# Kernel tuning notes

Measured on AMD Instinct MI355X. Metric: run time of the kernel, lower is better.

Reference implementation:

```python
import jax, jax.numpy as jnp
import numpy as np

N = 100000      # nodes
E = 1600000     # edges (avg degree 16)
IN, H, OUT = 128, 128, 64


def setup_inputs() -> dict:
    key = jax.random.key(0)
    ks = jax.random.split(key, 6)
    x = jax.random.normal(ks[0], (N, IN), dtype=jnp.float32)
    edge_index = jax.random.randint(ks[1], (2, E), 0, N, dtype=jnp.int64)
    # normalize=False => adj_t values hold precomputed GCN norm weights
    edge_weight = jax.random.uniform(ks[2], (E,), dtype=jnp.float32)

    def glorot(k, fi, fo):
        lim = np.sqrt(6.0 / (fi + fo)).astype(np.float32)
        return jax.random.uniform(k, (fi, fo), jnp.float32, -lim, lim)

    W1, b1 = glorot(ks[3], IN, H), jnp.zeros((H,), jnp.float32)
    W2, b2 = glorot(ks[4], H, H), jnp.zeros((H,), jnp.float32)
    W3, b3 = glorot(ks[5], H, OUT), jnp.zeros((OUT,), jnp.float32)
    return {"x": x, "edge_index": edge_index, "edge_weight": edge_weight,
            "W1": W1, "b1": b1, "W2": W2, "b2": b2, "W3": W3, "b3": b3}


def _gcn_conv(x, W, b, src, dst, w):
    # GCNConv(normalize=False): linear transform then weighted scatter-sum (adj_t @ h)
    h = x @ W                                    # [N, F_out]
    msg = h[src] * w[:, None]                    # gather + weight, [E, F_out]
    agg = jax.ops.segment_sum(msg, dst, num_segments=N)
    return agg + b


def reference(x, edge_index, edge_weight, W1, b1, W2, b2, W3, b3):
    src, dst = edge_index[0], edge_index[1]
    h = jax.nn.relu(_gcn_conv(x, W1, b1, src, dst, edge_weight))
    # dropout is identity at inference (training=False)
    h = jax.nn.relu(_gcn_conv(h, W2, b2, src, dst, edge_weight))
    return _gcn_conv(h, W3, b3, src, dst, edge_weight)
```

## Files before the change

kernel.cpp:

```cpp
#include <hip/hip_runtime.h>


typedef __attribute__((ext_vector_type(8))) short short8;
typedef __attribute__((ext_vector_type(4))) float f32x4;

__device__ __forceinline__ unsigned short f2bf(float f) {
  union { float f; unsigned u; } v; v.f = f;
  unsigned r = v.u + 0x7fffu + ((v.u >> 16) & 1u);
  return (unsigned short)(r >> 16);
}
__device__ __forceinline__ float bf2f(unsigned short h) {
  union { unsigned u; float f; } v; v.u = (unsigned)h << 16;
  return v.f;
}

constexpr int ABLK = 256;
constexpr int BINSHIFT = 8;
constexpr int MAXBINS = 512;
constexpr int SRCBITS = 17;
constexpr int SRCMASK = (1 << SRCBITS) - 1;

__global__ __launch_bounds__(256) void binhist_kernel(
    const int* __restrict__ dst, int* __restrict__ G, int E, int nbins,
    int chunk) {
  __shared__ int h[MAXBINS];
  for (int i = threadIdx.x; i < nbins; i += 256) h[i] = 0;
  __syncthreads();
  const int base = blockIdx.x * chunk;
  const int end = min(base + chunk, E);
  for (int i = base + threadIdx.x; i < end; i += 256)
    atomicAdd(&h[__builtin_nontemporal_load(dst + i) >> BINSHIFT], 1);
  __syncthreads();
  for (int i = threadIdx.x; i < nbins; i += 256)
    G[i * ABLK + blockIdx.x] = h[i];
}

__global__ __launch_bounds__(256) void scan_local_kernel(
    int* __restrict__ G, int* __restrict__ binTot) {
  __shared__ int sc[256];
  const int b = blockIdx.x;
  const int v = G[b * ABLK + threadIdx.x];
  sc[threadIdx.x] = v;
  __syncthreads();
  for (int off = 1; off < 256; off <<= 1) {
    const int mine = sc[threadIdx.x];
    const int add = (threadIdx.x >= off) ? sc[threadIdx.x - off] : 0;
    __syncthreads();
    sc[threadIdx.x] = mine + add;
    __syncthreads();
  }
  G[b * ABLK + threadIdx.x] = sc[threadIdx.x] - v;
  if (threadIdx.x == 255) binTot[b] = sc[255];
}

__global__ __launch_bounds__(256) void scan_bins_kernel(
    const int* __restrict__ binTot, int* __restrict__ binBase, int nbins,
    int E) {
  __shared__ int sc[512];
  sc[threadIdx.x] = (threadIdx.x < nbins) ? binTot[threadIdx.x] : 0;
  sc[threadIdx.x + 256] =
      (threadIdx.x + 256 < nbins) ? binTot[threadIdx.x + 256] : 0;
  for (int d = 1; d < 512; d <<= 1) {
    __syncthreads();
    const int idx = (threadIdx.x + 1) * (d << 1) - 1;
    if (idx < 512) sc[idx] += sc[idx - d];
  }
  __syncthreads();
  if (threadIdx.x == 0) sc[511] = 0;
  for (int d = 256; d >= 1; d >>= 1) {
    __syncthreads();
    const int idx = (threadIdx.x + 1) * (d << 1) - 1;
    if (idx < 512) {
      const int tmp = sc[idx - d];
      sc[idx - d] = sc[idx];
      sc[idx] += tmp;
    }
  }
  __syncthreads();
  if (threadIdx.x < nbins) binBase[threadIdx.x] = sc[threadIdx.x];
  if (threadIdx.x + 256 < nbins) binBase[threadIdx.x + 256] = sc[threadIdx.x + 256];
  if (threadIdx.x == 0) binBase[nbins] = E;
}

__global__ __launch_bounds__(256) void binscatter_kernel(
    const int* __restrict__ src, const int* __restrict__ dst,
    const float* __restrict__ ew, const int* __restrict__ G,
    const int* __restrict__ binBase, int2* __restrict__ bsw, int E, int nbins,
    int chunk) {
  __shared__ int cur[MAXBINS];
  for (int i = threadIdx.x; i < nbins; i += 256)
    cur[i] = binBase[i] + G[i * ABLK + blockIdx.x];
  __syncthreads();
  const int base = blockIdx.x * chunk;
  const int end = min(base + chunk, E);
  for (int i = base + threadIdx.x; i < end; i += 256) {
    const int d = __builtin_nontemporal_load(dst + i);
    const int s = __builtin_nontemporal_load(src + i);
    const float w = __builtin_nontemporal_load(ew + i);
    const int p = atomicAdd(&cur[d >> BINSHIFT], 1);
    bsw[p] = make_int2(s | ((d & 255) << SRCBITS), __float_as_int(w));
  }
}

__global__ __launch_bounds__(256) void csrbuild_kernel(
    const long* __restrict__ bsw, const int* __restrict__ binBase,
    int* __restrict__ rowptr, int2* __restrict__ csr, int N, int E,
    int nbins) {
  constexpr int CAP = 6144;
  __shared__ long stage[CAP];
  __shared__ int deg[256];
  __shared__ int sc[256];
  const int b = blockIdx.x;
  const int node0 = b << BINSHIFT;
  const int beg = binBase[b];
  const int cnt = binBase[b + 1] - beg;
  const bool fit = (cnt <= CAP);

  deg[threadIdx.x] = 0;
  __syncthreads();
  for (int i = threadIdx.x; i < cnt; i += 256) {
    const long c = __builtin_nontemporal_load(bsw + beg + i);
    if (fit) stage[i] = c;
    atomicAdd(&deg[((int)c >> SRCBITS) & 255], 1);
  }
  __syncthreads();

  const int s = deg[threadIdx.x];
  sc[threadIdx.x] = s;
  __syncthreads();
  for (int off = 1; off < 256; off <<= 1) {
    const int mine = sc[threadIdx.x];
    const int add = (threadIdx.x >= off) ? sc[threadIdx.x - off] : 0;
    __syncthreads();
    sc[threadIdx.x] = mine + add;
    __syncthreads();
  }
  const int rp = beg + sc[threadIdx.x] - s;
  if (node0 + threadIdx.x < N) rowptr[node0 + threadIdx.x] = rp;
  deg[threadIdx.x] = rp;
  __syncthreads();
  for (int i = threadIdx.x; i < cnt; i += 256) {
    const long c = fit ? stage[i] : bsw[beg + i];
    const int lo = (int)c;
    const int p = atomicAdd(&deg[(lo >> SRCBITS) & 255], 1);
    csr[p] = make_int2(lo & SRCMASK, (int)(c >> 32));
  }
  if (b == 0 && threadIdx.x == 0) rowptr[N] = E;
}

__global__ __launch_bounds__(256) void prep_w_kernel(
    const float* __restrict__ W1, const float* __restrict__ W2,
    const float* __restrict__ W3, unsigned short* __restrict__ WT1,
    unsigned short* __restrict__ WT2, unsigned short* __restrict__ WT3) {
  const int id = blockIdx.x * 256 + threadIdx.x;
  const float* W;
  unsigned short* WT;
  int NC, idx;
  if (id < 16384) { W = W1; WT = WT1; NC = 128; idx = id; }
  else if (id < 32768) { W = W2; WT = WT2; NC = 128; idx = id - 16384; }
  else if (id < 40960) { W = W3; WT = WT3; NC = 64; idx = id - 32768; }
  else return;
  const int k = idx / NC, n = idx % NC;
  *(unsigned short*)((char*)WT + n * 256 + ((2 * k) ^ ((n & 7) << 4))) =
      f2bf(W[idx]);
}

template <int NC, bool IN_F32>
__global__ __launch_bounds__(256) void gemm_mfma_kernel(
    const void* __restrict__ in, const unsigned short* __restrict__ WT,
    unsigned short* __restrict__ outp, int nrows) {
  constexpr int NT = NC / 16;
  __shared__ unsigned short Wlds[NC * 128];
  {
    const float4* wsrc = (const float4*)WT;
    float4* wdst = (float4*)Wlds;
    for (int i = threadIdx.x; i < NC * 256 / 16; i += 256) wdst[i] = wsrc[i];
  }
  __syncthreads();

  const int lane = threadIdx.x & 63;
  const int wave = threadIdx.x >> 6;
  const int nl = lane & 15;
  const int kl = (lane >> 4) * 8;
  const int rb = blockIdx.x * 64 + wave * 16;
  const int ra = min(rb + nl, nrows - 1);
  const int swz = (nl & 7) << 4;
  const char* wbase = (const char*)Wlds + nl * 256;

  f32x4 acc[NT] = {};

#pragma unroll
  for (int k0 = 0; k0 < 128; k0 += 32) {
    short8 a;
    if (IN_F32) {
      const float* xp = (const float*)in + (size_t)ra * 128 + k0 + kl;
      const float4 x0 = *(const float4*)xp;
      const float4 x1 = *(const float4*)(xp + 4);
      a[0] = (short)f2bf(x0.x); a[1] = (short)f2bf(x0.y);
      a[2] = (short)f2bf(x0.z); a[3] = (short)f2bf(x0.w);
      a[4] = (short)f2bf(x1.x); a[5] = (short)f2bf(x1.y);
      a[6] = (short)f2bf(x1.z); a[7] = (short)f2bf(x1.w);
    } else {
      a = *(const short8*)((const unsigned short*)in + (size_t)ra * 128 + k0 + kl);
    }
    const int koff = (2 * (k0 + kl)) ^ swz;
#pragma unroll
    for (int ct = 0; ct < NT; ++ct) {
      const short8 b = *(const short8*)(wbase + ct * 4096 + koff);
      acc[ct] = __builtin_amdgcn_mfma_f32_16x16x32_bf16(a, b, acc[ct], 0, 0, 0);
    }
  }

  const int r0 = rb + (lane >> 4) * 4;
#pragma unroll
  for (int ct = 0; ct < NT; ++ct) {
#pragma unroll
    for (int j = 0; j < 4; ++j) {
      const int r = r0 + j;
      if (r < nrows) outp[(size_t)r * NC + ct * 16 + nl] = f2bf(acc[ct][j]);
    }
  }
}

template <bool BF16OUT>
__global__ __launch_bounds__(256) void gather128_kernel(
    const unsigned short* __restrict__ t, const long* __restrict__ csr,
    const int* __restrict__ rowptr, const float* __restrict__ bias,
    void* __restrict__ outp, int n) {
  const int lane = threadIdx.x & 63;
  const int node = blockIdx.x * 4 + (threadIdx.x >> 6);
  if (node >= n) return;
  const int beg = __builtin_amdgcn_readfirstlane(rowptr[node]);
  const int end = __builtin_amdgcn_readfirstlane(rowptr[node + 1]);

  float2 ac[8];
  ac[0] = *(const float2*)&bias[lane * 2];
#pragma unroll
  for (int j = 1; j < 8; ++j) ac[j] = {0.f, 0.f};

  int e = beg;
  for (; e + 8 <= end; e += 8) {
    long c[8];
#pragma unroll
    for (int j = 0; j < 8; ++j) c[j] = __builtin_nontemporal_load(csr + e + j);
    unsigned v[8];
#pragma unroll
    for (int j = 0; j < 8; ++j)
      v[j] = *(const unsigned*)&t[(size_t)(int)c[j] * 128 + lane * 2];
#pragma unroll
    for (int j = 0; j < 8; ++j) {
      const float w = __int_as_float((int)(c[j] >> 32));
      ac[j].x = fmaf(bf2f((unsigned short)v[j]), w, ac[j].x);
      ac[j].y = fmaf(bf2f((unsigned short)(v[j] >> 16)), w, ac[j].y);
    }
  }
  for (; e < end; ++e) {
    const long c = __builtin_nontemporal_load(csr + e);
    const unsigned v = *(const unsigned*)&t[(size_t)(int)c * 128 + lane * 2];
    const float w = __int_as_float((int)(c >> 32));
    ac[0].x = fmaf(bf2f((unsigned short)v), w, ac[0].x);
    ac[0].y = fmaf(bf2f((unsigned short)(v >> 16)), w, ac[0].y);
  }
#pragma unroll
  for (int j = 1; j < 8; ++j) {
    ac[0].x += ac[j].x;
    ac[0].y += ac[j].y;
  }
  if (BF16OUT) {
    ac[0].x = fmaxf(ac[0].x, 0.f);
    ac[0].y = fmaxf(ac[0].y, 0.f);
    const unsigned pk = (unsigned)f2bf(ac[0].x) | ((unsigned)f2bf(ac[0].y) << 16);
    *(unsigned*)((unsigned short*)outp + (size_t)node * 128 + lane * 2) = pk;
  } else {
    *(float2*)((float*)outp + (size_t)node * 128 + lane * 2) = ac[0];
  }
}

__device__ __forceinline__ void acc_edge64(const unsigned short* t, long c,
                                           int ql, float4& a) {
  const int s = (int)c;
  const float w = __int_as_float((int)(c >> 32));
  const uint2 v = *(const uint2*)&t[(size_t)s * 64 + ql * 4];
  a.x = fmaf(bf2f((unsigned short)v.x), w, a.x);
  a.y = fmaf(bf2f((unsigned short)(v.x >> 16)), w, a.y);
  a.z = fmaf(bf2f((unsigned short)v.y), w, a.z);
  a.w = fmaf(bf2f((unsigned short)(v.y >> 16)), w, a.w);
}

__global__ __launch_bounds__(256) void gather64_kernel(
    const unsigned short* __restrict__ t, const long* __restrict__ csr,
    const int* __restrict__ rowptr, const float* __restrict__ bias,
    float* __restrict__ outp, int n) {
  const int wave = threadIdx.x >> 6;
  const int q = (threadIdx.x >> 4) & 3;
  const int ql = threadIdx.x & 15;
  const int node = blockIdx.x * 16 + wave * 4 + q;
  if (node >= n) return;
  int e = rowptr[node];
  const int end = rowptr[node + 1];

  float4 a0 = *(const float4*)&bias[ql * 4];
  float4 a1 = {0, 0, 0, 0}, a2 = {0, 0, 0, 0}, a3 = {0, 0, 0, 0};
  for (; e + 4 <= end; e += 4) {
    const long c0 = __builtin_nontemporal_load(csr + e);
    const long c1 = __builtin_nontemporal_load(csr + e + 1);
    const long c2 = __builtin_nontemporal_load(csr + e + 2);
    const long c3 = __builtin_nontemporal_load(csr + e + 3);
    acc_edge64(t, c0, ql, a0);
    acc_edge64(t, c1, ql, a1);
    acc_edge64(t, c2, ql, a2);
    acc_edge64(t, c3, ql, a3);
  }
  for (; e < end; ++e)
    acc_edge64(t, __builtin_nontemporal_load(csr + e), ql, a0);
  a0.x += a1.x + a2.x + a3.x;
  a0.y += a1.y + a2.y + a3.y;
  a0.z += a1.z + a2.z + a3.z;
  a0.w += a1.w + a2.w + a3.w;
  *(float4*)&outp[(size_t)node * 64 + ql * 4] = a0;
}

extern "C" void kernel_launch(void* const* d_in, const int* in_sizes, int n_in,
                              void* d_out, int out_size, void* d_ws, size_t ws_size,
                              hipStream_t stream) {
  const float* x  = (const float*)d_in[0];
  const int*   ei = (const int*)d_in[1];
  const float* ew = (const float*)d_in[2];
  const float* W1 = (const float*)d_in[3];
  const float* b1 = (const float*)d_in[4];
  const float* W2 = (const float*)d_in[5];
  const float* b2 = (const float*)d_in[6];
  const float* W3 = (const float*)d_in[7];
  const float* b3 = (const float*)d_in[8];

  const int E = in_sizes[2];
  const int N = in_sizes[0] / 128;
  const int* src = ei;
  const int* dst = ei + E;

  const int nbins = (N + 255) >> BINSHIFT;
  const int chunk = (E + ABLK - 1) / ABLK;

  unsigned short* WT1 = (unsigned short*)d_ws;
  unsigned short* WT2 = WT1 + 16384;
  unsigned short* WT3 = WT2 + 16384;
  unsigned short* t = WT3 + 8192;
  unsigned short* g = t + (size_t)N * 128;
  int2* csr = (int2*)(g + (size_t)N * 128);
  int* rowptr = (int*)(csr + E);
  int* G = rowptr + (N + 1);
  int* binTot = G + nbins * ABLK;
  int* binBase = binTot + nbins;
  int2* bsw = (int2*)g;

  const int gemm_blocks = (N + 63) / 64;
  const int g128_blocks = (N + 3) / 4;
  const int g64_blocks = (N + 15) / 16;

  prep_w_kernel<<<160, 256, 0, stream>>>(W1, W2, W3, WT1, WT2, WT3);
  binhist_kernel<<<ABLK, 256, 0, stream>>>(dst, G, E, nbins, chunk);
  scan_local_kernel<<<nbins, 256, 0, stream>>>(G, binTot);
  scan_bins_kernel<<<1, 256, 0, stream>>>(binTot, binBase, nbins, E);
  binscatter_kernel<<<ABLK, 256, 0, stream>>>(src, dst, ew, G, binBase, bsw,
                                              E, nbins, chunk);
  csrbuild_kernel<<<nbins, 256, 0, stream>>>((const long*)bsw, binBase,
                                             rowptr, csr, N, E, nbins);

  gemm_mfma_kernel<128, true><<<gemm_blocks, 256, 0, stream>>>(x, WT1, t, N);
  gather128_kernel<true><<<g128_blocks, 256, 0, stream>>>(
      t, (const long*)csr, rowptr, b1, g, N);

  gemm_mfma_kernel<128, false><<<gemm_blocks, 256, 0, stream>>>(g, WT2, t, N);
  gather128_kernel<true><<<g128_blocks, 256, 0, stream>>>(
      t, (const long*)csr, rowptr, b2, g, N);

  gemm_mfma_kernel<64, false><<<gemm_blocks, 256, 0, stream>>>(g, WT3, t, N);
  gather64_kernel<<<g64_blocks, 256, 0, stream>>>(
      t, (const long*)csr, rowptr, b3, (float*)d_out, N);
}
```

Measured before the change: 271.6 us.

## Fuse gather-aggregate with the following layer's GEMM via LDS staging

Replaces the separate gather128 and gemm kernels for layers 2 and 3 with one fused kernel. Each block aggregates 64 node rows into a swizzled LDS tile (bias plus ReLU, bf16) and multiplies that tile by the next layer's weights, also loaded into LDS, using MFMA. This avoids writing the aggregated features to global memory and reading them back, and removes two launches. In exchange each wave gathers 16 nodes one after another and the block must finish gathering before it synchronises, which lowers latency hiding and occupancy given the larger LDS footprint.

```diff
diff --git a/kernel.cpp b/kernel.cpp
--- a/kernel.cpp
+++ b/kernel.cpp
@@ -222,57 +222,99 @@
   }
 }
 
-template <bool BF16OUT>
-__global__ __launch_bounds__(256) void gather128_kernel(
+template <int NC>
+__global__ __launch_bounds__(256) void fused_gather_gemm_kernel(
     const unsigned short* __restrict__ t, const long* __restrict__ csr,
     const int* __restrict__ rowptr, const float* __restrict__ bias,
-    void* __restrict__ outp, int n) {
+    const unsigned short* __restrict__ WT, unsigned short* __restrict__ outp,
+    int n) {
+  constexpr int NT = NC / 16;
+  __shared__ unsigned short Wlds[NC * 128];
+  __shared__ unsigned short Glds[64 * 128];
+  {
+    const float4* wsrc = (const float4*)WT;
+    float4* wdst = (float4*)Wlds;
+    for (int i = threadIdx.x; i < NC * 256 / 16; i += 256) wdst[i] = wsrc[i];
+  }
+
   const int lane = threadIdx.x & 63;
-  const int node = blockIdx.x * 4 + (threadIdx.x >> 6);
-  if (node >= n) return;
-  const int beg = __builtin_amdgcn_readfirstlane(rowptr[node]);
-  const int end = __builtin_amdgcn_readfirstlane(rowptr[node + 1]);
-
-  float2 ac[8];
-  ac[0] = *(const float2*)&bias[lane * 2];
-#pragma unroll
-  for (int j = 1; j < 8; ++j) ac[j] = {0.f, 0.f};
-
-  int e = beg;
-  for (; e + 8 <= end; e += 8) {
-    long c[8];
-#pragma unroll
-    for (int j = 0; j < 8; ++j) c[j] = __builtin_nontemporal_load(csr + e + j);
-    unsigned v[8];
-#pragma unroll
-    for (int j = 0; j < 8; ++j)
-      v[j] = *(const unsigned*)&t[(size_t)(int)c[j] * 128 + lane * 2];
-#pragma unroll
-    for (int j = 0; j < 8; ++j) {
-      const float w = __int_as_float((int)(c[j] >> 32));
-      ac[j].x = fmaf(bf2f((unsigned short)v[j]), w, ac[j].x);
-      ac[j].y = fmaf(bf2f((unsigned short)(v[j] >> 16)), w, ac[j].y);
-    }
-  }
-  for (; e < end; ++e) {
-    const long c = __builtin_nontemporal_load(csr + e);
-    const unsigned v = *(const unsigned*)&t[(size_t)(int)c * 128 + lane * 2];
-    const float w = __int_as_float((int)(c >> 32));
-    ac[0].x = fmaf(bf2f((unsigned short)v), w, ac[0].x);
-    ac[0].y = fmaf(bf2f((unsigned short)(v >> 16)), w, ac[0].y);
-  }
-#pragma unroll
-  for (int j = 1; j < 8; ++j) {
-    ac[0].x += ac[j].x;
-    ac[0].y += ac[j].y;
-  }
-  if (BF16OUT) {
+  const int wave = threadIdx.x >> 6;
+  const int base = blockIdx.x * 64;
+
+  for (int it = 0; it < 16; ++it) {
+    const int r = it * 4 + wave;
+    const int node = base + r;
+    unsigned* rowp =
+        (unsigned*)((char*)Glds + r * 256 + ((lane * 4) ^ ((r & 7) << 4)));
+    if (node >= n) { *rowp = 0; continue; }
+    const int beg = __builtin_amdgcn_readfirstlane(rowptr[node]);
+    const int end = __builtin_amdgcn_readfirstlane(rowptr[node + 1]);
+
+    float2 ac[8];
+    ac[0] = *(const float2*)&bias[lane * 2];
+#pragma unroll
+    for (int j = 1; j < 8; ++j) ac[j] = {0.f, 0.f};
+
+    int e = beg;
+    for (; e + 8 <= end; e += 8) {
+      long c[8];
+#pragma unroll
+      for (int j = 0; j < 8; ++j) c[j] = __builtin_nontemporal_load(csr + e + j);
+      unsigned v[8];
+#pragma unroll
+      for (int j = 0; j < 8; ++j)
+        v[j] = *(const unsigned*)&t[(size_t)(int)c[j] * 128 + lane * 2];
+#pragma unroll
+      for (int j = 0; j < 8; ++j) {
+        const float w = __int_as_float((int)(c[j] >> 32));
+        ac[j].x = fmaf(bf2f((unsigned short)v[j]), w, ac[j].x);
+        ac[j].y = fmaf(bf2f((unsigned short)(v[j] >> 16)), w, ac[j].y);
+      }
+    }
+    for (; e < end; ++e) {
+      const long c = __builtin_nontemporal_load(csr + e);
+      const unsigned v = *(const unsigned*)&t[(size_t)(int)c * 128 + lane * 2];
+      const float w = __int_as_float((int)(c >> 32));
+      ac[0].x = fmaf(bf2f((unsigned short)v), w, ac[0].x);
+      ac[0].y = fmaf(bf2f((unsigned short)(v >> 16)), w, ac[0].y);
+    }
+#pragma unroll
+    for (int j = 1; j < 8; ++j) {
+      ac[0].x += ac[j].x;
+      ac[0].y += ac[j].y;
+    }
     ac[0].x = fmaxf(ac[0].x, 0.f);
     ac[0].y = fmaxf(ac[0].y, 0.f);
-    const unsigned pk = (unsigned)f2bf(ac[0].x) | ((unsigned)f2bf(ac[0].y) << 16);
-    *(unsigned*)((unsigned short*)outp + (size_t)node * 128 + lane * 2) = pk;
-  } else {
-    *(float2*)((float*)outp + (size_t)node * 128 + lane * 2) = ac[0];
+    *rowp = (unsigned)f2bf(ac[0].x) | ((unsigned)f2bf(ac[0].y) << 16);
+  }
+  __syncthreads();
+
+  const int nl = lane & 15;
+  const int kl = (lane >> 4) * 8;
+  const int swz = (nl & 7) << 4;
+  const char* gbase = (const char*)Glds + (wave * 16 + nl) * 256;
+  const char* wbase = (const char*)Wlds + nl * 256;
+
+  f32x4 acc[NT] = {};
+#pragma unroll
+  for (int k0 = 0; k0 < 128; k0 += 32) {
+    const int koff = (2 * (k0 + kl)) ^ swz;
+    const short8 a = *(const short8*)(gbase + koff);
+#pragma unroll
+    for (int ct = 0; ct < NT; ++ct) {
+      const short8 b = *(const short8*)(wbase + ct * 4096 + koff);
+      acc[ct] = __builtin_amdgcn_mfma_f32_16x16x32_bf16(a, b, acc[ct], 0, 0, 0);
+    }
+  }
+
+  const int r0 = base + wave * 16 + (lane >> 4) * 4;
+#pragma unroll
+  for (int ct = 0; ct < NT; ++ct) {
+#pragma unroll
+    for (int j = 0; j < 4; ++j) {
+      const int r = r0 + j;
+      if (r < n) outp[(size_t)r * NC + ct * 16 + nl] = f2bf(acc[ct][j]);
+    }
   }
 }
 
@@ -354,7 +396,7 @@
   int2* bsw = (int2*)g;
 
   const int gemm_blocks = (N + 63) / 64;
-  const int g128_blocks = (N + 3) / 4;
+  const int fused_blocks = (N + 63) / 64;
   const int g64_blocks = (N + 15) / 16;
 
   prep_w_kernel<<<160, 256, 0, stream>>>(W1, W2, W3, WT1, WT2, WT3);
@@ -367,14 +409,13 @@
                                              rowptr, csr, N, E, nbins);
 
   gemm_mfma_kernel<128, true><<<gemm_blocks, 256, 0, stream>>>(x, WT1, t, N);
-  gather128_kernel<true><<<g128_blocks, 256, 0, stream>>>(
-      t, (const long*)csr, rowptr, b1, g, N);
-
-  gemm_mfma_kernel<128, false><<<gemm_blocks, 256, 0, stream>>>(g, WT2, t, N);
-  gather128_kernel<true><<<g128_blocks, 256, 0, stream>>>(
-      t, (const long*)csr, rowptr, b2, g, N);
-
-  gemm_mfma_kernel<64, false><<<gemm_blocks, 256, 0, stream>>>(g, WT3, t, N);
+
+  fused_gather_gemm_kernel<128><<<fused_blocks, 256, 0, stream>>>(
+      t, (const long*)csr, rowptr, b1, WT2, g, N);
+
+  fused_gather_gemm_kernel<64><<<fused_blocks, 256, 0, stream>>>(
+      g, (const long*)csr, rowptr, b2, WT3, t, N);
+
   gather64_kernel<<<g64_blocks, 256, 0, stream>>>(
       t, (const long*)csr, rowptr, b3, (float*)d_out, N);
 }
```

New measurement: 363.1 us. 1.34x slower.
